# Performance work log

Measured on AMD Instinct MI355X. Metric: run time of the kernel, lower is better.

The kernel has to match this reference:

```python
import jax, jax.numpy as jnp
import numpy as np

N_FFT = 1024
HOP = 256
WIN = 1024
SIG_LEN = 16777216  # 2**24 samples


def _hamming_sym(M):
    # scipy.signal.hamming(M, sym=True): 0.54 - 0.46*cos(2*pi*n/(M-1))
    n = np.arange(M)
    return (0.54 - 0.46 * np.cos(2.0 * np.pi * n / (M - 1))).astype(np.float32)


def setup_inputs() -> dict:
    key = jax.random.key(0)
    x = jax.random.normal(key, (SIG_LEN,), dtype=jnp.float32)
    return {"x": x}


def reference(x):
    # window, normalized by sqrt(n_fft) (sum of Hamming window is nonzero)
    win = jnp.asarray(_hamming_sym(WIN) / np.sqrt(N_FFT).astype(np.float32))
    hw2 = WIN // 2
    half_n = N_FFT // 2 + 1
    pad = 3 * HOP

    xp = jnp.pad(x, (pad, pad))       # np.append zeros on both sides
    total = xp.shape[0]
    n_rows = total // HOP             # allocated output rows (trailing rows stay zero)
    n_frames = (total - WIN) // HOP + 1  # frames actually computed by the while-loop

    starts = jnp.arange(n_frames) * HOP
    frames = xp[starts[:, None] + jnp.arange(WIN)[None, :]] * win

    # zero-phase buffer: buf[:hw1] = win_x[hw2:], buf[-hw2:] = win_x[:hw2]
    mid = jnp.zeros((n_frames, N_FFT - WIN), dtype=frames.dtype)
    buf = jnp.concatenate([frames[:, hw2:], mid, frames[:, :hw2]], axis=1)

    spec = jnp.fft.rfft(buf, n=N_FFT, axis=1)        # [n_frames, half_n] complex64
    mag = jnp.abs(spec).astype(jnp.float32)
    ph = jnp.angle(spec).astype(jnp.float32)

    xm_x = jnp.zeros((n_rows, half_n), jnp.float32).at[:n_frames].set(mag)
    xp_x = jnp.zeros((n_rows, half_n), jnp.float32).at[:n_frames].set(ph)
    return (xm_x, xp_x)
```

## Files before the change

kernel.cpp:

```cpp
#include <hip/hip_runtime.h>


#define SIG_LEN   16777216
#define N_FRAMES  65539
#define N_ROWS    65542
#define HALF_N    513
#define FRAMES_FLOATS (N_FRAMES * HALF_N)
#define MAG_SZ        (N_ROWS   * HALF_N)


__global__ void init_tables(double* __restrict__ ws) {
  int i = blockIdx.x * 256 + threadIdx.x;
  const double PI = 3.14159265358979323846;
  if (i < 1024) {
    ws[i] = (0.54 - 0.46 * cos(2.0 * PI * (double)i / 1023.0)) / 32.0;
  }
  if (i < 256) {
    double a = -2.0 * PI * (double)i / 512.0;
    ws[1024 + 2 * i]     = cos(a);
    ws[1024 + 2 * i + 1] = sin(a);
  }
  if (i < 513) {
    double a = -2.0 * PI * (double)i / 1024.0;
    ws[1536 + 2 * i]     = cos(a);
    ws[1536 + 2 * i + 1] = sin(a);
  }
}

__global__ void zero_tail(float* __restrict__ out) {
  int i = blockIdx.x * 256 + threadIdx.x;
  if (i < (MAG_SZ - FRAMES_FLOATS)) {
    out[FRAMES_FLOATS + i] = 0.0f;
    out[MAG_SZ + FRAMES_FLOATS + i] = 0.0f;
  }
}

#define PAD(e) ((e) + ((e) >> 3) + ((e) >> 6))

#define CMUL(vr, vi, wx, wy) { double _t = (vr)*(wx) - (vi)*(wy); \
                               (vi) = (vr)*(wy) + (vi)*(wx); (vr) = _t; }

__device__ __forceinline__ void dft8(double* ar, double* ai) {
  const double S = 0.70710678118654752440;
  double s0r = ar[0] + ar[4], s0i = ai[0] + ai[4];
  double s1r = ar[0] - ar[4], s1i = ai[0] - ai[4];
  double s2r = ar[2] + ar[6], s2i = ai[2] + ai[6];
  double s3r = ar[2] - ar[6], s3i = ai[2] - ai[6];
  double t0r = ar[1] + ar[5], t0i = ai[1] + ai[5];
  double t1r = ar[1] - ar[5], t1i = ai[1] - ai[5];
  double t2r = ar[3] + ar[7], t2i = ai[3] + ai[7];
  double t3r = ar[3] - ar[7], t3i = ai[3] - ai[7];

  double e0r = s0r + s2r, e0i = s0i + s2i;
  double e2r = s0r - s2r, e2i = s0i - s2i;
  double e1r = s1r + s3i, e1i = s1i - s3r;
  double e3r = s1r - s3i, e3i = s1i + s3r;
  double o0r = t0r + t2r, o0i = t0i + t2i;
  double o2r = t0r - t2r, o2i = t0i - t2i;
  double o1r = t1r + t3i, o1i = t1i - t3r;
  double o3r = t1r - t3i, o3i = t1i + t3r;

  double u1r = S * (o1r + o1i), u1i = S * (o1i - o1r);
  double u2r = o2i,             u2i = -o2r;
  double u3r = S * (o3i - o3r), u3i = -S * (o3r + o3i);

  ar[0] = e0r + o0r; ai[0] = e0i + o0i;
  ar[4] = e0r - o0r; ai[4] = e0i - o0i;
  ar[1] = e1r + u1r; ai[1] = e1i + u1i;
  ar[5] = e1r - u1r; ai[5] = e1i - u1i;
  ar[2] = e2r + u2r; ai[2] = e2i + u2i;
  ar[6] = e2r - u2r; ai[6] = e2i - u2i;
  ar[3] = e3r + u3r; ai[3] = e3i + u3i;
  ar[7] = e3r - u3r; ai[7] = e3i - u3i;
}

__device__ __forceinline__ void twmul(double* ar, double* ai, double wx, double wy) {
  double px = wx, py = wy;
  CMUL(ar[1], ai[1], px, py);
#pragma unroll
  for (int r = 2; r < 8; ++r) {
    double nx = px * wx - py * wy;
    double ny = px * wy + py * wx;
    px = nx; py = ny;
    CMUL(ar[r], ai[r], px, py);
  }
}

__global__ __launch_bounds__(256) void stft_frame(const float* __restrict__ x,
                                                  const double* __restrict__ ws,
                                                  float* __restrict__ out) {
  __shared__ double2 zbuf[4][584];

  const int wv = threadIdx.x >> 6;
  const int l  = threadIdx.x & 63;
  const int f  = blockIdx.x * 4 + wv;
  if (f >= N_FRAMES) return;
  double2* z = zbuf[wv];

  double ar[8], ai[8];
  const int base = f * 256 - 768;
#pragma unroll
  for (int n2 = 0; n2 < 8; ++n2) {
    int j  = 128 * n2 + 2 * l;
    int ix = base + j;
    double v0, v1;
    if (ix >= 0 && ix + 1 < SIG_LEN) {
      float2 xv = *(const float2*)(x + ix);
      v0 = (double)xv.x; v1 = (double)xv.y;
    } else {
      v0 = (ix >= 0 && ix < SIG_LEN) ? (double)x[ix] : 0.0;
      v1 = (ix + 1 >= 0 && ix + 1 < SIG_LEN) ? (double)x[ix + 1] : 0.0;
    }
    double2 wn = *(const double2*)(ws + j);
    ar[n2] = v0 * wn.x;
    ai[n2] = v1 * wn.y;
  }

  const int g = l >> 3;
  const int q = l & 7;

  dft8(ar, ai);
  {
    double2 w = ((const double2*)(ws + 1024))[l];
    twmul(ar, ai, w.x, w.y);
  }

#pragma unroll
  for (int r = 0; r < 8; ++r) {
    int e = 64 * r + l;
    z[PAD(e)] = make_double2(ar[r], ai[r]);
  }
  asm volatile("s_waitcnt lgkmcnt(0)" ::: "memory");
#pragma unroll
  for (int r = 0; r < 8; ++r) {
    int e = 64 * g + 8 * r + q;
    double2 v = z[PAD(e)];
    ar[r] = v.x; ai[r] = v.y;
  }

  dft8(ar, ai);
  {
    double2 w = ((const double2*)(ws + 1024))[8 * q];
    twmul(ar, ai, w.x, w.y);
  }

#pragma unroll
  for (int r = 0; r < 8; ++r) {
    int e = 64 * g + 8 * r + q;
    z[PAD(e)] = make_double2(ar[r], ai[r]);
  }
  asm volatile("s_waitcnt lgkmcnt(0)" ::: "memory");
#pragma unroll
  for (int r = 0; r < 8; ++r) {
    int e = 64 * g + 8 * q + r;
    double2 v = z[PAD(e)];
    ar[r] = v.x; ai[r] = v.y;
  }

  dft8(ar, ai);

#pragma unroll
  for (int r = 0; r < 8; ++r) {
    int e = 64 * r + 8 * q + g;
    z[PAD(e)] = make_double2(ar[r], ai[r]);
  }
  asm volatile("s_waitcnt lgkmcnt(0)" ::: "memory");

  const double2* rtw = (const double2*)(ws + 1536);
  for (int k = l; k < HALF_N; k += 64) {
    double2 Zk = z[PAD(k & 511)];
    double2 Zm = z[PAD((512 - k) & 511)];
    double Er = 0.5 * (Zk.x + Zm.x);
    double Ei = 0.5 * (Zk.y - Zm.y);
    double Or = 0.5 * (Zk.y + Zm.y);
    double Oi = -0.5 * (Zk.x - Zm.x);
    double2 w = rtw[k];
    double Yr = Er + w.x * Or - w.y * Oi;
    double Yi = Ei + w.x * Oi + w.y * Or;
    if ((k & 511) == 0) Yi = 0.0;
    float yr = (float)Yr;
    float yi = (float)Yi;
    float mag = sqrtf(yr * yr + yi * yi);
    float pr = (k & 1) ? -yr : yr;
    float pi = (k & 1) ? -yi : yi;
    float ph = atan2f(pi, pr);
    out[f * HALF_N + k] = mag;
    out[MAG_SZ + f * HALF_N + k] = ph;
  }
}

extern "C" void kernel_launch(void* const* d_in, const int* in_sizes, int n_in,
                              void* d_out, int out_size, void* d_ws, size_t ws_size,
                              hipStream_t stream) {
  const float* x = (const float*)d_in[0];
  float* out = (float*)d_out;
  double* ws = (double*)d_ws;

  hipLaunchKernelGGL(init_tables, dim3(4), dim3(256), 0, stream, ws);
  hipLaunchKernelGGL(zero_tail, dim3(7), dim3(256), 0, stream, out);
  hipLaunchKernelGGL(stft_frame, dim3((N_FRAMES + 3) / 4), dim3(256), 0, stream,
                     x, ws, out);
}
```

Before: 441.5 us.

## Precompute per-lane twiddles, XOR-swizzle LDS, and fold real-FFT post-processing into tables

Replaces the on-the-fly twiddle power recurrence with precomputed per-lane twiddle tables for both radix-8 stages. Swaps the padded LDS layout for XOR-swizzled indexing. Recasts the real-FFT split step as a product with precomputed A/B coefficients, with the Nyquist bin handled separately. Also adds a fast unguarded load path for interior frames and an occupancy hint in the launch bounds. The aim is to cut FP64 ALU work and LDS bank conflicts, at the cost of more global table loads.

Result: faster. 403.5 us (-8.6%).

```diff
diff --git a/kernel.cpp b/kernel.cpp
--- a/kernel.cpp
+++ b/kernel.cpp
@@ -15,15 +15,25 @@
   if (i < 1024) {
     ws[i] = (0.54 - 0.46 * cos(2.0 * PI * (double)i / 1023.0)) / 32.0;
   }
-  if (i < 256) {
-    double a = -2.0 * PI * (double)i / 512.0;
+  if (i < 448) {
+    int l = i / 7, r = i % 7 + 1;
+    double a = -2.0 * PI * (double)(l * r) / 512.0;
     ws[1024 + 2 * i]     = cos(a);
     ws[1024 + 2 * i + 1] = sin(a);
   }
+  if (i < 56) {
+    int q = i / 7, r = i % 7 + 1;
+    double a = -2.0 * PI * (double)(8 * q * r) / 512.0;
+    ws[1920 + 2 * i]     = cos(a);
+    ws[1920 + 2 * i + 1] = sin(a);
+  }
   if (i < 513) {
-    double a = -2.0 * PI * (double)i / 1024.0;
-    ws[1536 + 2 * i]     = cos(a);
-    ws[1536 + 2 * i + 1] = sin(a);
+    double th = PI * (double)i / 512.0;
+    double c = cos(th), s = sin(th);
+    ws[2048 + 4 * i]     = 0.5 * (1.0 - s);
+    ws[2048 + 4 * i + 1] = -0.5 * c;
+    ws[2048 + 4 * i + 2] = 0.5 * (1.0 + s);
+    ws[2048 + 4 * i + 3] = 0.5 * c;
   }
 }
 
@@ -34,8 +44,6 @@
     out[MAG_SZ + FRAMES_FLOATS + i] = 0.0f;
   }
 }
-
-#define PAD(e) ((e) + ((e) >> 3) + ((e) >> 6))
 
 #define CMUL(vr, vi, wx, wy) { double _t = (vr)*(wx) - (vi)*(wy); \
                                (vi) = (vr)*(wy) + (vi)*(wx); (vr) = _t; }
@@ -74,22 +82,10 @@
   ar[7] = e3r - u3r; ai[7] = e3i - u3i;
 }
 
-__device__ __forceinline__ void twmul(double* ar, double* ai, double wx, double wy) {
-  double px = wx, py = wy;
-  CMUL(ar[1], ai[1], px, py);
-#pragma unroll
-  for (int r = 2; r < 8; ++r) {
-    double nx = px * wx - py * wy;
-    double ny = px * wy + py * wx;
-    px = nx; py = ny;
-    CMUL(ar[r], ai[r], px, py);
-  }
-}
-
-__global__ __launch_bounds__(256) void stft_frame(const float* __restrict__ x,
-                                                  const double* __restrict__ ws,
-                                                  float* __restrict__ out) {
-  __shared__ double2 zbuf[4][584];
+__global__ __launch_bounds__(256, 5) void stft_frame(const float* __restrict__ x,
+                                                     const double* __restrict__ ws,
+                                                     float* __restrict__ out) {
+  __shared__ double2 zbuf[4][512];
 
   const int wv = threadIdx.x >> 6;
   const int l  = threadIdx.x & 63;
@@ -97,63 +93,72 @@
   if (f >= N_FRAMES) return;
   double2* z = zbuf[wv];
 
+  const int g = l >> 3;
+  const int q = l & 7;
+
   double ar[8], ai[8];
   const int base = f * 256 - 768;
-#pragma unroll
-  for (int n2 = 0; n2 < 8; ++n2) {
-    int j  = 128 * n2 + 2 * l;
-    int ix = base + j;
-    double v0, v1;
-    if (ix >= 0 && ix + 1 < SIG_LEN) {
-      float2 xv = *(const float2*)(x + ix);
-      v0 = (double)xv.x; v1 = (double)xv.y;
-    } else {
-      v0 = (ix >= 0 && ix < SIG_LEN) ? (double)x[ix] : 0.0;
-      v1 = (ix + 1 >= 0 && ix + 1 < SIG_LEN) ? (double)x[ix + 1] : 0.0;
-    }
-    double2 wn = *(const double2*)(ws + j);
-    ar[n2] = v0 * wn.x;
-    ai[n2] = v1 * wn.y;
-  }
-
-  const int g = l >> 3;
-  const int q = l & 7;
+  if (base >= 0 && base + 1024 <= SIG_LEN) {
+#pragma unroll
+    for (int n2 = 0; n2 < 8; ++n2) {
+      int j = 128 * n2 + 2 * l;
+      float2 xv = *(const float2*)(x + base + j);
+      double2 wn = *(const double2*)(ws + j);
+      ar[n2] = (double)xv.x * wn.x;
+      ai[n2] = (double)xv.y * wn.y;
+    }
+  } else {
+#pragma unroll
+    for (int n2 = 0; n2 < 8; ++n2) {
+      int j  = 128 * n2 + 2 * l;
+      int ix = base + j;
+      double v0 = (ix >= 0 && ix < SIG_LEN) ? (double)x[ix] : 0.0;
+      double v1 = (ix + 1 >= 0 && ix + 1 < SIG_LEN) ? (double)x[ix + 1] : 0.0;
+      double2 wn = *(const double2*)(ws + j);
+      ar[n2] = v0 * wn.x;
+      ai[n2] = v1 * wn.y;
+    }
+  }
 
   dft8(ar, ai);
   {
-    double2 w = ((const double2*)(ws + 1024))[l];
-    twmul(ar, ai, w.x, w.y);
-  }
-
-#pragma unroll
-  for (int r = 0; r < 8; ++r) {
-    int e = 64 * r + l;
-    z[PAD(e)] = make_double2(ar[r], ai[r]);
+    const double2* tw1 = (const double2*)(ws + 1024) + l * 7;
+#pragma unroll
+    for (int r = 1; r < 8; ++r) {
+      double2 w = tw1[r - 1];
+      CMUL(ar[r], ai[r], w.x, w.y);
+    }
+  }
+
+#pragma unroll
+  for (int r = 0; r < 8; ++r) {
+    z[64 * r + 8 * g + (q ^ g)] = make_double2(ar[r], ai[r]);
   }
   asm volatile("s_waitcnt lgkmcnt(0)" ::: "memory");
 #pragma unroll
   for (int r = 0; r < 8; ++r) {
-    int e = 64 * g + 8 * r + q;
-    double2 v = z[PAD(e)];
+    double2 v = z[64 * g + 8 * r + (q ^ r)];
     ar[r] = v.x; ai[r] = v.y;
   }
 
   dft8(ar, ai);
   {
-    double2 w = ((const double2*)(ws + 1024))[8 * q];
-    twmul(ar, ai, w.x, w.y);
-  }
-
-#pragma unroll
-  for (int r = 0; r < 8; ++r) {
-    int e = 64 * g + 8 * r + q;
-    z[PAD(e)] = make_double2(ar[r], ai[r]);
+    const double2* tw2 = (const double2*)(ws + 1920) + q * 7;
+#pragma unroll
+    for (int r = 1; r < 8; ++r) {
+      double2 w = tw2[r - 1];
+      CMUL(ar[r], ai[r], w.x, w.y);
+    }
+  }
+
+#pragma unroll
+  for (int r = 0; r < 8; ++r) {
+    z[64 * g + 8 * r + (q ^ r)] = make_double2(ar[r], ai[r]);
   }
   asm volatile("s_waitcnt lgkmcnt(0)" ::: "memory");
 #pragma unroll
   for (int r = 0; r < 8; ++r) {
-    int e = 64 * g + 8 * q + r;
-    double2 v = z[PAD(e)];
+    double2 v = z[64 * g + 8 * q + (r ^ q)];
     ar[r] = v.x; ai[r] = v.y;
   }
 
@@ -161,31 +166,39 @@
 
 #pragma unroll
   for (int r = 0; r < 8; ++r) {
-    int e = 64 * r + 8 * q + g;
-    z[PAD(e)] = make_double2(ar[r], ai[r]);
+    z[64 * r + 8 * q + (g ^ q)] = make_double2(ar[r], ai[r]);
   }
   asm volatile("s_waitcnt lgkmcnt(0)" ::: "memory");
 
-  const double2* rtw = (const double2*)(ws + 1536);
-  for (int k = l; k < HALF_N; k += 64) {
-    double2 Zk = z[PAD(k & 511)];
-    double2 Zm = z[PAD((512 - k) & 511)];
-    double Er = 0.5 * (Zk.x + Zm.x);
-    double Ei = 0.5 * (Zk.y - Zm.y);
-    double Or = 0.5 * (Zk.y + Zm.y);
-    double Oi = -0.5 * (Zk.x - Zm.x);
-    double2 w = rtw[k];
-    double Yr = Er + w.x * Or - w.y * Oi;
-    double Yi = Ei + w.x * Oi + w.y * Or;
-    if ((k & 511) == 0) Yi = 0.0;
+  const double* AB = ws + 2048;
+  const int czk = 8 * (l >> 3) + ((l & 7) ^ (l >> 3));
+  const float sgn = (l & 1) ? -1.0f : 1.0f;
+#pragma unroll
+  for (int i = 0; i < 8; ++i) {
+    int k = l + 64 * i;
+    double2 Zk = z[64 * i + czk];
+    int km = (512 - k) & 511;
+    double2 Zm = z[(km & ~7) | ((km ^ (km >> 3)) & 7)];
+    const double* ab = AB + 4 * k;
+    double Axv = ab[0], Ayv = ab[1], Bxv = ab[2], Byv = ab[3];
+    double Yr = Zk.x * Axv - Zk.y * Ayv + Zm.x * Bxv + Zm.y * Byv;
+    double Yi = Zk.x * Ayv + Zk.y * Axv + Zm.x * Byv - Zm.y * Bxv;
+    if (i == 0 && l == 0) Yi = 0.0;
     float yr = (float)Yr;
     float yi = (float)Yi;
     float mag = sqrtf(yr * yr + yi * yi);
-    float pr = (k & 1) ? -yr : yr;
-    float pi = (k & 1) ? -yi : yi;
-    float ph = atan2f(pi, pr);
+    float ph = atan2f(sgn * yi, sgn * yr);
     out[f * HALF_N + k] = mag;
     out[MAG_SZ + f * HALF_N + k] = ph;
+  }
+
+  if (l == 0) {
+    double2 z0 = z[0];
+    double Yr = z0.x - z0.y;
+    float yr = (float)Yr;
+    out[f * HALF_N + 512] = fabsf(yr);
+    out[MAG_SZ + f * HALF_N + 512] =
+        __builtin_signbitf(yr) ? 3.14159265358979323846f : 0.0f;
   }
 }
 
```
